# Optimization experiments

Measured on AMD Instinct MI355X. Metric: run time of the kernel, lower is better.

The kernel has to match this reference:

```python
import jax, jax.numpy as jnp
import numpy as np

N_NODES = 1_000_000
N_EDGES = 16_000_000
NUM_REL = 3
C_IN, C_OUT = 3, 2


def setup_inputs() -> dict:
    key = jax.random.key(0)
    ks = jax.random.split(key, 10)
    x = jax.random.normal(ks[0], (N_NODES, C_IN), dtype=jnp.float32)
    edge_index = jax.random.randint(ks[1], (2, N_EDGES), 0, N_NODES, dtype=jnp.int64)
    edge_attr = jax.random.randint(ks[2], (N_EDGES,), 0, NUM_REL, dtype=jnp.int64)
    s = 0.3
    W1 = jax.random.normal(ks[3], (NUM_REL, C_IN, C_OUT), dtype=jnp.float32) * s
    root1 = jax.random.normal(ks[4], (C_IN, C_OUT), dtype=jnp.float32) * s
    b1 = jax.random.normal(ks[5], (C_OUT,), dtype=jnp.float32) * s
    W2 = jax.random.normal(ks[6], (NUM_REL, C_OUT, C_OUT), dtype=jnp.float32) * s
    root2 = jax.random.normal(ks[7], (C_OUT, C_OUT), dtype=jnp.float32) * s
    b2 = jax.random.normal(ks[8], (C_OUT,), dtype=jnp.float32) * s
    return {"x": x, "edge_index": edge_index, "edge_attr": edge_attr,
            "W1": W1, "root1": root1, "b1": b1,
            "W2": W2, "root2": root2, "b2": b2}


def rgcn_conv(x, edge_index, edge_type, W, root, bias, num_nodes):
    """PyG RGCNConv: per-relation mean-aggregated messages + root transform + bias."""
    src, dst = edge_index[0], edge_index[1]
    xs = x[src]                                    # [E, c_in] gather once
    out = x @ root + bias                          # [N, c_out]
    for r in range(NUM_REL):                       # small fixed relation loop
        mask = (edge_type == r)
        msg = jnp.where(mask[:, None], xs @ W[r], 0.0)          # [E, c_out]
        sums = jax.ops.segment_sum(msg, dst, num_segments=num_nodes)
        cnt = jax.ops.segment_sum(mask.astype(x.dtype), dst, num_segments=num_nodes)
        out = out + sums / jnp.maximum(cnt, 1.0)[:, None]       # mean aggr
    return out


def reference(x, edge_index, edge_attr, W1, root1, b1, W2, root2, b2):
    h = rgcn_conv(x, edge_index, edge_attr, W1, root1, b1, N_NODES)
    h = jax.nn.relu(h)
    # F.dropout(training=self.training): identity in eval mode
    out = rgcn_conv(h, edge_index, edge_attr, W2, root2, b2, N_NODES)
    return out
```

## Files before the change

### kernel.cpp

```cpp
#include <hip/hip_runtime.h>


typedef unsigned long long u64;
typedef unsigned u32;

constexpr int NN = 1000000;
constexpr int NE = 16000000;
constexpr int NR = 3;

constexpr int BSH   = 10;
constexpr int NB    = (NN + 1023) >> 10;
constexpr int BCAP  = 18432;
constexpr int EPB   = 16384;
constexpr int NBLKB = (NE + EPB - 1) / EPB;

__device__ __forceinline__ u32 enc_x(float x0, float x1, float x2) {
    int q0 = __float2int_rn(fminf(fmaxf(x0 * 64.0f, -511.0f), 511.0f));
    int q1 = __float2int_rn(fminf(fmaxf(x1 * 128.0f, -1023.0f), 1023.0f));
    int q2 = __float2int_rn(fminf(fmaxf(x2 * 128.0f, -1023.0f), 1023.0f));
    return ((u32)(q0 + 512) & 0x3FFu)
         | (((u32)(q1 + 1024) & 0x7FFu) << 10)
         | (((u32)(q2 + 1024) & 0x7FFu) << 21);
}

__device__ __forceinline__ u64 widen_x(u32 q) {
    return (u64)(q & 0x3FFu)
         | ((u64)((q >> 10) & 0x7FFu) << 18)
         | ((u64)(q >> 21) << 36)
         | (1ULL << 54);
}

__device__ __forceinline__ u32 enc_h(float h0, float h1) {
    int q0 = __float2int_rn(fminf(h0 * 1024.0f, 32767.0f));
    int q1 = __float2int_rn(fminf(h1 * 1024.0f, 32767.0f));
    return ((u32)q0 & 0xFFFFu) | ((u32)q1 << 16);
}

__device__ __forceinline__ u64 widen_h(u32 q) {
    return (u64)(q & 0xFFFFu)
         | ((u64)(q >> 16) << 22)
         | (1ULL << 44);
}

__device__ __forceinline__ void dec_h(u32 e, float& h0, float& h1) {
    h0 = (float)(e & 0xFFFFu) * (1.0f / 1024.0f);
    h1 = (float)(e >> 16)     * (1.0f / 1024.0f);
}

constexpr u64 M28 = (1ULL << 28) - 1;
__device__ __forceinline__ u64 pack_msg(float m0, float m1) {
    int a0 = __float2int_rn(fmaf(m0, 4096.0f, 524288.0f));
    int a1 = __float2int_rn(fmaf(m1, 4096.0f, 524288.0f));
    return (u64)(u32)a0 | ((u64)(u32)a1 << 28) | (1ULL << 56);
}


__global__ __launch_bounds__(1024, 8) void scatter_kernel(
    const int* __restrict__ src, const int* __restrict__ dst, const int* __restrict__ rel,
    const float* __restrict__ x, u32* __restrict__ qx,
    u32* __restrict__ buf, u32* __restrict__ cursor)
{
    __shared__ u32 stage[EPB];
    __shared__ u32 hist[1024];
    __shared__ u32 wcur[1024];
    __shared__ u32 gbase[1024];
    __shared__ u32 wt[16];
    const int tid = threadIdx.x;
    const int wave = tid >> 6, lane = tid & 63;

    {
        int node = blockIdx.x * 1024 + tid;
        if (node < NN)
            qx[node] = enc_x(x[3 * node + 0], x[3 * node + 1], x[3 * node + 2]);
    }

    hist[tid] = 0;
    __syncthreads();

    const int base = blockIdx.x * EPB;
    const int nloc = min(EPB, NE - base);
    const int g4 = nloc >> 2;
    const int4* dp = (const int4*)(dst + base);
    const int4* sp = (const int4*)(src + base);
    const int4* rp = (const int4*)(rel + base);

    {
        const int i0 = tid, i1 = tid + 1024, i2 = tid + 2048, i3 = tid + 3072;
        const bool v0 = i0 < g4, v1 = i1 < g4, v2 = i2 < g4, v3 = i3 < g4;
        int4 a0, a1, a2, a3;
        if (v0) a0 = dp[i0];
        if (v1) a1 = dp[i1];
        if (v2) a2 = dp[i2];
        if (v3) a3 = dp[i3];
        if (v0) {
            atomicAdd(&hist[((u32)a0.x) >> BSH], 1u);
            atomicAdd(&hist[((u32)a0.y) >> BSH], 1u);
            atomicAdd(&hist[((u32)a0.z) >> BSH], 1u);
            atomicAdd(&hist[((u32)a0.w) >> BSH], 1u);
        }
        if (v1) {
            atomicAdd(&hist[((u32)a1.x) >> BSH], 1u);
            atomicAdd(&hist[((u32)a1.y) >> BSH], 1u);
            atomicAdd(&hist[((u32)a1.z) >> BSH], 1u);
            atomicAdd(&hist[((u32)a1.w) >> BSH], 1u);
        }
        if (v2) {
            atomicAdd(&hist[((u32)a2.x) >> BSH], 1u);
            atomicAdd(&hist[((u32)a2.y) >> BSH], 1u);
            atomicAdd(&hist[((u32)a2.z) >> BSH], 1u);
            atomicAdd(&hist[((u32)a2.w) >> BSH], 1u);
        }
        if (v3) {
            atomicAdd(&hist[((u32)a3.x) >> BSH], 1u);
            atomicAdd(&hist[((u32)a3.y) >> BSH], 1u);
            atomicAdd(&hist[((u32)a3.z) >> BSH], 1u);
            atomicAdd(&hist[((u32)a3.w) >> BSH], 1u);
        }
    }
    __syncthreads();

    {
        int h0 = hist[tid];
        int v0 = h0;
#pragma unroll
        for (int d = 1; d < 64; d <<= 1) {
            int t = __shfl_up(v0, d);
            if (lane >= d) v0 += t;
        }
        if (lane == 63) wt[wave] = (u32)v0;
        __syncthreads();
        u32 off = 0;
#pragma unroll
        for (int wv = 0; wv < 16; ++wv) off += (wv < wave) ? wt[wv] : 0u;
        wcur[tid] = off + (u32)(v0 - h0);
    }
    __syncthreads();

    if (tid < NB) {
        u32 c = hist[tid];
        gbase[tid] = c ? atomicAdd(&cursor[tid], c) : 0u;
    }
    __syncthreads();

    for (int i = tid; i < g4; i += 2048) {
        const int j = i + 1024;
        const bool vj = j < g4;
        int4 d0 = dp[i], s0 = sp[i], r0 = rp[i];
        int4 d1, s1, r1;
        if (vj) { d1 = dp[j]; s1 = sp[j]; r1 = rp[j]; }
        {
            u32 dd = (u32)d0.x, bk = dd >> BSH;
            u32 sl = atomicAdd(&wcur[bk], 1u);
            stage[sl] = (u32)s0.x | ((u32)r0.x << 20) | ((dd & 1023u) << 22);
        }
        {
            u32 dd = (u32)d0.y, bk = dd >> BSH;
            u32 sl = atomicAdd(&wcur[bk], 1u);
            stage[sl] = (u32)s0.y | ((u32)r0.y << 20) | ((dd & 1023u) << 22);
        }
        {
            u32 dd = (u32)d0.z, bk = dd >> BSH;
            u32 sl = atomicAdd(&wcur[bk], 1u);
            stage[sl] = (u32)s0.z | ((u32)r0.z << 20) | ((dd & 1023u) << 22);
        }
        {
            u32 dd = (u32)d0.w, bk = dd >> BSH;
            u32 sl = atomicAdd(&wcur[bk], 1u);
            stage[sl] = (u32)s0.w | ((u32)r0.w << 20) | ((dd & 1023u) << 22);
        }
        if (vj) {
            {
                u32 dd = (u32)d1.x, bk = dd >> BSH;
                u32 sl = atomicAdd(&wcur[bk], 1u);
                stage[sl] = (u32)s1.x | ((u32)r1.x << 20) | ((dd & 1023u) << 22);
            }
            {
                u32 dd = (u32)d1.y, bk = dd >> BSH;
                u32 sl = atomicAdd(&wcur[bk], 1u);
                stage[sl] = (u32)s1.y | ((u32)r1.y << 20) | ((dd & 1023u) << 22);
            }
            {
                u32 dd = (u32)d1.z, bk = dd >> BSH;
                u32 sl = atomicAdd(&wcur[bk], 1u);
                stage[sl] = (u32)s1.z | ((u32)r1.z << 20) | ((dd & 1023u) << 22);
            }
            {
                u32 dd = (u32)d1.w, bk = dd >> BSH;
                u32 sl = atomicAdd(&wcur[bk], 1u);
                stage[sl] = (u32)s1.w | ((u32)r1.w << 20) | ((dd & 1023u) << 22);
            }
        }
    }
    __syncthreads();

    {
        const int sub = lane >> 4;
        const int l16 = lane & 15;
        for (int b = (wave << 2) + sub; b < NB; b += 64) {
            u32 cnt = hist[b];
            if (!cnt) continue;
            u32 ls = wcur[b] - cnt;
            u32 gb = gbase[b];
            u32* bb = buf + (size_t)b * BCAP;
            for (u32 j = l16; j < cnt; j += 16) {
                u32 slot = gb + j;
                if (slot < (u32)BCAP) bb[slot] = stage[ls + j];
            }
        }
    }
}

__global__ __launch_bounds__(512) void agg1_kernel(
    const u32* __restrict__ buf, const u32* __restrict__ cursor,
    const u32* __restrict__ qx, const float* __restrict__ x,
    const float* __restrict__ W1,
    const float* __restrict__ root1, const float* __restrict__ b1,
    u32* __restrict__ qh)
{
    __shared__ u64 acc[1024 * NR];
    __shared__ float w[NR * 3 * 2];
    const int tid = threadIdx.x;
    for (int i = tid; i < 1024 * NR; i += 512) acc[i] = 0;
    if (tid < NR * 3 * 2) w[tid] = W1[tid];
    __syncthreads();

    const int bk = blockIdx.x;
    const int n = min((int)cursor[bk], BCAP);
    const u32* bb = buf + (size_t)bk * BCAP;
    const int n8 = n >> 3;

    int g = tid;
    uint4 A0 = make_uint4(0, 0, 0, 0), A1 = A0;
    if (g < n8) {
        const uint4* p = (const uint4*)(bb + ((size_t)g << 3));
        A0 = p[0]; A1 = p[1];
    }
    while (g < n8) {
        const int gn = g + 512;
        uint4 B0 = make_uint4(0, 0, 0, 0), B1 = B0;
        if (gn < n8) {
            const uint4* p = (const uint4*)(bb + ((size_t)gn << 3));
            B0 = p[0]; B1 = p[1];
        }
        u32 e[8] = {A0.x, A0.y, A0.z, A0.w, A1.x, A1.y, A1.z, A1.w};
        u32 q[8];
#pragma unroll
        for (int j = 0; j < 8; ++j) q[j] = qx[e[j] & 0xFFFFFu];
#pragma unroll
        for (int j = 0; j < 8; ++j)
            atomicAdd(&acc[(e[j] >> 22) * NR + ((e[j] >> 20) & 3u)], widen_x(q[j]));
        A0 = B0; A1 = B1; g = gn;
    }
    for (int i = (n8 << 3) + tid; i < n; i += 512) {
        u32 e0 = bb[i];
        u32 q0 = qx[e0 & 0xFFFFFu];
        atomicAdd(&acc[(e0 >> 22) * NR + ((e0 >> 20) & 3u)], widen_x(q0));
    }
    __syncthreads();

    for (int l = tid; l < 1024; l += 512) {
        int node = (bk << BSH) + l;
        if (node >= NN) continue;
        float x0 = x[3 * node + 0], x1 = x[3 * node + 1], x2 = x[3 * node + 2];
        float o0 = x0 * root1[0] + x1 * root1[2] + x2 * root1[4] + b1[0];
        float o1 = x0 * root1[1] + x1 * root1[3] + x2 * root1[5] + b1[1];
#pragma unroll
        for (int r = 0; r < NR; ++r) {
            u64 wv = acc[l * NR + r];
            u32 c = (u32)(wv >> 54);
            if (c) {
                float inv = 1.0f / (float)c;
                float S0 = (float)(u32)(wv & 0x3FFFFu);
                float S1 = (float)(u32)((wv >> 18) & 0x3FFFFu);
                float S2 = (float)(u32)((wv >> 36) & 0x3FFFFu);
                float m0 = fmaf(S0, inv, -512.0f)  * (1.0f / 64.0f);
                float m1 = fmaf(S1, inv, -1024.0f) * (1.0f / 128.0f);
                float m2 = fmaf(S2, inv, -1024.0f) * (1.0f / 128.0f);
                const float* wr = &w[r * 6];
                o0 += m0 * wr[0] + m1 * wr[2] + m2 * wr[4];
                o1 += m0 * wr[1] + m1 * wr[3] + m2 * wr[5];
            }
        }
        qh[node] = enc_h(fmaxf(o0, 0.0f), fmaxf(o1, 0.0f));
    }
}

__global__ __launch_bounds__(512) void agg2_kernel(
    const u32* __restrict__ buf, const u32* __restrict__ cursor,
    const u32* __restrict__ qh, const float* __restrict__ W2,
    const float* __restrict__ root2, const float* __restrict__ b2,
    float* __restrict__ out)
{
    __shared__ u64 acc[1024 * NR];
    __shared__ float w[NR * 2 * 2];
    const int tid = threadIdx.x;
    for (int i = tid; i < 1024 * NR; i += 512) acc[i] = 0;
    if (tid < NR * 2 * 2) w[tid] = W2[tid];
    __syncthreads();

    const int bk = blockIdx.x;
    const int n = min((int)cursor[bk], BCAP);
    const u32* bb = buf + (size_t)bk * BCAP;
    const int n8 = n >> 3;

    int g = tid;
    uint4 A0 = make_uint4(0, 0, 0, 0), A1 = A0;
    if (g < n8) {
        const uint4* p = (const uint4*)(bb + ((size_t)g << 3));
        A0 = p[0]; A1 = p[1];
    }
    while (g < n8) {
        const int gn = g + 512;
        uint4 B0 = make_uint4(0, 0, 0, 0), B1 = B0;
        if (gn < n8) {
            const uint4* p = (const uint4*)(bb + ((size_t)gn << 3));
            B0 = p[0]; B1 = p[1];
        }
        u32 e[8] = {A0.x, A0.y, A0.z, A0.w, A1.x, A1.y, A1.z, A1.w};
        u32 q[8];
#pragma unroll
        for (int j = 0; j < 8; ++j) q[j] = qh[e[j] & 0xFFFFFu];
#pragma unroll
        for (int j = 0; j < 8; ++j)
            atomicAdd(&acc[(e[j] >> 22) * NR + ((e[j] >> 20) & 3u)], widen_h(q[j]));
        A0 = B0; A1 = B1; g = gn;
    }
    for (int i = (n8 << 3) + tid; i < n; i += 512) {
        u32 e0 = bb[i];
        u32 q0 = qh[e0 & 0xFFFFFu];
        atomicAdd(&acc[(e0 >> 22) * NR + ((e0 >> 20) & 3u)], widen_h(q0));
    }
    __syncthreads();

    for (int l = tid; l < 1024; l += 512) {
        int node = (bk << BSH) + l;
        if (node >= NN) continue;
        float hv0, hv1;
        dec_h(qh[node], hv0, hv1);
        float o0 = hv0 * root2[0] + hv1 * root2[2] + b2[0];
        float o1 = hv0 * root2[1] + hv1 * root2[3] + b2[1];
#pragma unroll
    for (int r = 0; r < NR; ++r) {
            u64 wv = acc[l * NR + r];
            u32 c = (u32)(wv >> 44);
            if (c) {
                float inv = 1.0f / (float)c;
                float m0 = (float)(u32)(wv & 0x3FFFFFu)         * inv * (1.0f / 1024.0f);
                float m1 = (float)(u32)((wv >> 22) & 0x3FFFFFu) * inv * (1.0f / 1024.0f);
                const float* wr = &w[r * 4];
                o0 += m0 * wr[0] + m1 * wr[2];
                o1 += m0 * wr[1] + m1 * wr[3];
            }
        }
        float2 ov; ov.x = o0; ov.y = o1;
        ((float2*)out)[node] = ov;
    }
}


__global__ __launch_bounds__(256) void edge1_kernel(
    const int* __restrict__ src, const int* __restrict__ dst, const int* __restrict__ rel,
    const float* __restrict__ x, const float* __restrict__ W1,
    u64* __restrict__ sums1)
{
    __shared__ float w[NR * 3 * 2];
    if (threadIdx.x < NR * 3 * 2) w[threadIdx.x] = W1[threadIdx.x];
    __syncthreads();
    int e = blockIdx.x * 256 + threadIdx.x;
    if (e >= NE) return;
    int s = src[e], d = dst[e], r = rel[e];
    float x0 = x[3 * s + 0], x1 = x[3 * s + 1], x2 = x[3 * s + 2];
    const float* wr = &w[r * 6];
    float m0 = x0 * wr[0] + x1 * wr[2] + x2 * wr[4];
    float m1 = x0 * wr[1] + x1 * wr[3] + x2 * wr[5];
    atomicAdd(&sums1[d * NR + r], pack_msg(m0, m1));
}

__global__ __launch_bounds__(256) void node1_kernel(
    const float* __restrict__ x, const u64* __restrict__ sums1,
    const float* __restrict__ root1, const float* __restrict__ b1,
    float* __restrict__ h)
{
    int n = blockIdx.x * 256 + threadIdx.x;
    if (n >= NN) return;
    float x0 = x[3 * n + 0], x1 = x[3 * n + 1], x2 = x[3 * n + 2];
    float o0 = x0 * root1[0] + x1 * root1[2] + x2 * root1[4] + b1[0];
    float o1 = x0 * root1[1] + x1 * root1[3] + x2 * root1[5] + b1[1];
#pragma unroll
    for (int r = 0; r < NR; ++r) {
        u64 wv = sums1[n * NR + r];
        int c = (int)(wv >> 56);
        int s0i = (int)(wv & M28) - (c << 19);
        int s1i = (int)((wv >> 28) & M28) - (c << 19);
        float inv = (1.0f / 4096.0f) / (float)(c > 1 ? c : 1);
        o0 += (float)s0i * inv;
        o1 += (float)s1i * inv;
    }
    float2 hv;
    hv.x = fmaxf(o0, 0.0f);
    hv.y = fmaxf(o1, 0.0f);
    ((float2*)h)[n] = hv;
}

__global__ __launch_bounds__(256) void edge2_kernel(
    const int* __restrict__ src, const int* __restrict__ dst, const int* __restrict__ rel,
    const float* __restrict__ h, const float* __restrict__ W2,
    u64* __restrict__ sums2)
{
    __shared__ float w[NR * 2 * 2];
    if (threadIdx.x < NR * 2 * 2) w[threadIdx.x] = W2[threadIdx.x];
    __syncthreads();
    int e = blockIdx.x * 256 + threadIdx.x;
    if (e >= NE) return;
    int s = src[e];
    float2 hs = ((const float2*)h)[s];
    if (hs.x == 0.0f && hs.y == 0.0f) return;
    int d = dst[e], r = rel[e];
    const float* wr = &w[r * 4];
    float m0 = hs.x * wr[0] + hs.y * wr[2];
    float m1 = hs.x * wr[1] + hs.y * wr[3];
    atomicAdd(&sums2[d * NR + r], pack_msg(m0, m1));
}

__global__ __launch_bounds__(256) void node2_kernel(
    const float* __restrict__ h, const u64* __restrict__ sums1, const u64* __restrict__ sums2,
    const float* __restrict__ root2, const float* __restrict__ b2,
    float* __restrict__ out)
{
    int n = blockIdx.x * 256 + threadIdx.x;
    if (n >= NN) return;
    float2 hv = ((const float2*)h)[n];
    float o0 = hv.x * root2[0] + hv.y * root2[2] + b2[0];
    float o1 = hv.x * root2[1] + hv.y * root2[3] + b2[1];
#pragma unroll
    for (int r = 0; r < NR; ++r) {
        u64 w1 = sums1[n * NR + r];
        u64 w2 = sums2[n * NR + r];
        int c    = (int)(w1 >> 56);
        int adds = (int)(w2 >> 56);
        int s0i = (int)(w2 & M28) - (adds << 19);
        int s1i = (int)((w2 >> 28) & M28) - (adds << 19);
        float inv = (1.0f / 4096.0f) / (float)(c > 1 ? c : 1);
        o0 += (float)s0i * inv;
        o1 += (float)s1i * inv;
    }
    float2 ov; ov.x = o0; ov.y = o1;
    ((float2*)out)[n] = ov;
}

extern "C" void kernel_launch(void* const* d_in, const int* in_sizes, int n_in,
                              void* d_out, int out_size, void* d_ws, size_t ws_size,
                              hipStream_t stream) {
    const float* x     = (const float*)d_in[0];
    const int*   ei    = (const int*)d_in[1];
    const int*   rel   = (const int*)d_in[2];
    const float* W1    = (const float*)d_in[3];
    const float* root1 = (const float*)d_in[4];
    const float* b1    = (const float*)d_in[5];
    const float* W2    = (const float*)d_in[6];
    const float* root2 = (const float*)d_in[7];
    const float* b2    = (const float*)d_in[8];
    float* out = (float*)d_out;

    const int* src = ei;
    const int* dst = ei + NE;

    char* ws = (char*)d_ws;
    const int nb = (NN + 255) / 256;

    const size_t OFF_QX  = 72024064;
    const size_t OFF_QH  = 76024064;
    const size_t OFF_CUR = 80024064;
    const size_t WS_NEED = OFF_CUR + (size_t)NB * sizeof(u32);

    if (ws_size >= WS_NEED) {
        u32* buf    = (u32*)ws;
        u32* qx     = (u32*)(ws + OFF_QX);
        u32* qh     = (u32*)(ws + OFF_QH);
        u32* cursor = (u32*)(ws + OFF_CUR);

        hipMemsetAsync(cursor, 0, (size_t)NB * sizeof(u32), stream);
        scatter_kernel<<<NBLKB, 1024, 0, stream>>>(src, dst, rel, x, qx, buf, cursor);
        agg1_kernel<<<NB, 512, 0, stream>>>(buf, cursor, qx, x, W1, root1, b1, qh);
        agg2_kernel<<<NB, 512, 0, stream>>>(buf, cursor, qh, W2, root2, b2, out);
    } else {
        u64*   sums1 = (u64*)ws;
        u64*   sums2 = (u64*)(ws + (size_t)24 * 1000 * 1000);
        float* h     = (float*)(ws + (size_t)48 * 1000 * 1000);
        const int eb = (NE + 255) / 256;

        hipMemsetAsync(sums1, 0, (size_t)NN * NR * sizeof(u64), stream);
        hipMemsetAsync(sums2, 0, (size_t)NN * NR * sizeof(u64), stream);
        edge1_kernel<<<eb, 256, 0, stream>>>(src, dst, rel, x, W1, sums1);
        node1_kernel<<<nb, 256, 0, stream>>>(x, sums1, root1, b1, h);
        edge2_kernel<<<eb, 256, 0, stream>>>(src, dst, rel, h, W2, sums2);
        node2_kernel<<<nb, 256, 0, stream>>>(h, sums1, sums2, root2, b2, out);
    }
}
```

Before: 455.8 us.

## Fuse both aggregation layers into one kernel with a global grid barrier

Merges agg1 and agg2 into one persistent-style kernel. Each of the 977 blocks handles its bucket for layer 1, writes qh, then waits on a global atomic counter until every block has finished before running layer 2 on the same bucket. This removes one kernel launch and its launch gap. It relies on all NB blocks being resident at once (launch_bounds 512,8 plus 24KB of LDS per block), and it risks deadlock or a long spin wait if they are not.

```diff
diff --git a/kernel.cpp b/kernel.cpp
--- a/kernel.cpp
+++ b/kernel.cpp
@@ -210,51 +210,56 @@
     }
 }
 
-__global__ __launch_bounds__(512) void agg1_kernel(
+__global__ __launch_bounds__(512, 8) void fused_agg_kernel(
     const u32* __restrict__ buf, const u32* __restrict__ cursor,
     const u32* __restrict__ qx, const float* __restrict__ x,
     const float* __restrict__ W1,
     const float* __restrict__ root1, const float* __restrict__ b1,
-    u32* __restrict__ qh)
+    u32* __restrict__ qh,
+    const float* __restrict__ W2,
+    const float* __restrict__ root2, const float* __restrict__ b2,
+    float* __restrict__ out, u32* done)
 {
     __shared__ u64 acc[1024 * NR];
     __shared__ float w[NR * 3 * 2];
     const int tid = threadIdx.x;
-    for (int i = tid; i < 1024 * NR; i += 512) acc[i] = 0;
-    if (tid < NR * 3 * 2) w[tid] = W1[tid];
-    __syncthreads();
-
     const int bk = blockIdx.x;
     const int n = min((int)cursor[bk], BCAP);
     const u32* bb = buf + (size_t)bk * BCAP;
     const int n8 = n >> 3;
 
-    int g = tid;
-    uint4 A0 = make_uint4(0, 0, 0, 0), A1 = A0;
-    if (g < n8) {
-        const uint4* p = (const uint4*)(bb + ((size_t)g << 3));
-        A0 = p[0]; A1 = p[1];
-    }
-    while (g < n8) {
-        const int gn = g + 512;
-        uint4 B0 = make_uint4(0, 0, 0, 0), B1 = B0;
-        if (gn < n8) {
-            const uint4* p = (const uint4*)(bb + ((size_t)gn << 3));
-            B0 = p[0]; B1 = p[1];
-        }
-        u32 e[8] = {A0.x, A0.y, A0.z, A0.w, A1.x, A1.y, A1.z, A1.w};
-        u32 q[8];
-#pragma unroll
-        for (int j = 0; j < 8; ++j) q[j] = qx[e[j] & 0xFFFFFu];
-#pragma unroll
-        for (int j = 0; j < 8; ++j)
-            atomicAdd(&acc[(e[j] >> 22) * NR + ((e[j] >> 20) & 3u)], widen_x(q[j]));
-        A0 = B0; A1 = B1; g = gn;
-    }
-    for (int i = (n8 << 3) + tid; i < n; i += 512) {
-        u32 e0 = bb[i];
-        u32 q0 = qx[e0 & 0xFFFFFu];
-        atomicAdd(&acc[(e0 >> 22) * NR + ((e0 >> 20) & 3u)], widen_x(q0));
+    for (int i = tid; i < 1024 * NR; i += 512) acc[i] = 0;
+    if (tid < NR * 3 * 2) w[tid] = W1[tid];
+    __syncthreads();
+
+    {
+        int g = tid;
+        uint4 A0 = make_uint4(0, 0, 0, 0), A1 = A0;
+        if (g < n8) {
+            const uint4* p = (const uint4*)(bb + ((size_t)g << 3));
+            A0 = p[0]; A1 = p[1];
+        }
+        while (g < n8) {
+            const int gn = g + 512;
+            uint4 B0 = make_uint4(0, 0, 0, 0), B1 = B0;
+            if (gn < n8) {
+                const uint4* p = (const uint4*)(bb + ((size_t)gn << 3));
+                B0 = p[0]; B1 = p[1];
+            }
+            u32 e[8] = {A0.x, A0.y, A0.z, A0.w, A1.x, A1.y, A1.z, A1.w};
+            u32 q[8];
+#pragma unroll
+            for (int j = 0; j < 8; ++j) q[j] = qx[e[j] & 0xFFFFFu];
+#pragma unroll
+            for (int j = 0; j < 8; ++j)
+                atomicAdd(&acc[(e[j] >> 22) * NR + ((e[j] >> 20) & 3u)], widen_x(q[j]));
+            A0 = B0; A1 = B1; g = gn;
+        }
+        for (int i = (n8 << 3) + tid; i < n; i += 512) {
+            u32 e0 = bb[i];
+            u32 q0 = qx[e0 & 0xFFFFFu];
+            atomicAdd(&acc[(e0 >> 22) * NR + ((e0 >> 20) & 3u)], widen_x(q0));
+        }
     }
     __syncthreads();
 
@@ -283,52 +288,49 @@
         }
         qh[node] = enc_h(fmaxf(o0, 0.0f), fmaxf(o1, 0.0f));
     }
-}
-
-__global__ __launch_bounds__(512) void agg2_kernel(
-    const u32* __restrict__ buf, const u32* __restrict__ cursor,
-    const u32* __restrict__ qh, const float* __restrict__ W2,
-    const float* __restrict__ root2, const float* __restrict__ b2,
-    float* __restrict__ out)
-{
-    __shared__ u64 acc[1024 * NR];
-    __shared__ float w[NR * 2 * 2];
-    const int tid = threadIdx.x;
+
+    __syncthreads();
+    __threadfence();
+    if (tid == 0) {
+        atomicAdd(done, 1u);
+        while (__hip_atomic_load(done, __ATOMIC_ACQUIRE,
+                                 __HIP_MEMORY_SCOPE_AGENT) < (u32)NB) { }
+    }
+    __syncthreads();
+    __threadfence();
+
     for (int i = tid; i < 1024 * NR; i += 512) acc[i] = 0;
     if (tid < NR * 2 * 2) w[tid] = W2[tid];
     __syncthreads();
 
-    const int bk = blockIdx.x;
-    const int n = min((int)cursor[bk], BCAP);
-    const u32* bb = buf + (size_t)bk * BCAP;
-    const int n8 = n >> 3;
-
-    int g = tid;
-    uint4 A0 = make_uint4(0, 0, 0, 0), A1 = A0;
-    if (g < n8) {
-        const uint4* p = (const uint4*)(bb + ((size_t)g << 3));
-        A0 = p[0]; A1 = p[1];
-    }
-    while (g < n8) {
-        const int gn = g + 512;
-        uint4 B0 = make_uint4(0, 0, 0, 0), B1 = B0;
-        if (gn < n8) {
-            const uint4* p = (const uint4*)(bb + ((size_t)gn << 3));
-            B0 = p[0]; B1 = p[1];
-        }
-        u32 e[8] = {A0.x, A0.y, A0.z, A0.w, A1.x, A1.y, A1.z, A1.w};
-        u32 q[8];
-#pragma unroll
-        for (int j = 0; j < 8; ++j) q[j] = qh[e[j] & 0xFFFFFu];
-#pragma unroll
-        for (int j = 0; j < 8; ++j)
-            atomicAdd(&acc[(e[j] >> 22) * NR + ((e[j] >> 20) & 3u)], widen_h(q[j]));
-        A0 = B0; A1 = B1; g = gn;
-    }
-    for (int i = (n8 << 3) + tid; i < n; i += 512) {
-        u32 e0 = bb[i];
-        u32 q0 = qh[e0 & 0xFFFFFu];
-        atomicAdd(&acc[(e0 >> 22) * NR + ((e0 >> 20) & 3u)], widen_h(q0));
+    {
+        int g = tid;
+        uint4 A0 = make_uint4(0, 0, 0, 0), A1 = A0;
+        if (g < n8) {
+            const uint4* p = (const uint4*)(bb + ((size_t)g << 3));
+            A0 = p[0]; A1 = p[1];
+        }
+        while (g < n8) {
+            const int gn = g + 512;
+            uint4 B0 = make_uint4(0, 0, 0, 0), B1 = B0;
+            if (gn < n8) {
+                const uint4* p = (const uint4*)(bb + ((size_t)gn << 3));
+                B0 = p[0]; B1 = p[1];
+            }
+            u32 e[8] = {A0.x, A0.y, A0.z, A0.w, A1.x, A1.y, A1.z, A1.w};
+            u32 q[8];
+#pragma unroll
+            for (int j = 0; j < 8; ++j) q[j] = qh[e[j] & 0xFFFFFu];
+#pragma unroll
+            for (int j = 0; j < 8; ++j)
+                atomicAdd(&acc[(e[j] >> 22) * NR + ((e[j] >> 20) & 3u)], widen_h(q[j]));
+            A0 = B0; A1 = B1; g = gn;
+        }
+        for (int i = (n8 << 3) + tid; i < n; i += 512) {
+            u32 e0 = bb[i];
+            u32 q0 = qh[e0 & 0xFFFFFu];
+            atomicAdd(&acc[(e0 >> 22) * NR + ((e0 >> 20) & 3u)], widen_h(q0));
+        }
     }
     __syncthreads();
 
@@ -340,7 +342,7 @@
         float o0 = hv0 * root2[0] + hv1 * root2[2] + b2[0];
         float o1 = hv0 * root2[1] + hv1 * root2[3] + b2[1];
 #pragma unroll
-    for (int r = 0; r < NR; ++r) {
+        for (int r = 0; r < NR; ++r) {
             u64 wv = acc[l * NR + r];
             u32 c = (u32)(wv >> 44);
             if (c) {
@@ -471,18 +473,20 @@
     const size_t OFF_QX  = 72024064;
     const size_t OFF_QH  = 76024064;
     const size_t OFF_CUR = 80024064;
-    const size_t WS_NEED = OFF_CUR + (size_t)NB * sizeof(u32);
+    const size_t WS_NEED = OFF_CUR + (size_t)NB * sizeof(u32) + sizeof(u32);
 
     if (ws_size >= WS_NEED) {
         u32* buf    = (u32*)ws;
         u32* qx     = (u32*)(ws + OFF_QX);
         u32* qh     = (u32*)(ws + OFF_QH);
         u32* cursor = (u32*)(ws + OFF_CUR);
-
-        hipMemsetAsync(cursor, 0, (size_t)NB * sizeof(u32), stream);
+        u32* done   = cursor + NB;
+
+        hipMemsetAsync(cursor, 0, ((size_t)NB + 1) * sizeof(u32), stream);
         scatter_kernel<<<NBLKB, 1024, 0, stream>>>(src, dst, rel, x, qx, buf, cursor);
-        agg1_kernel<<<NB, 512, 0, stream>>>(buf, cursor, qx, x, W1, root1, b1, qh);
-        agg2_kernel<<<NB, 512, 0, stream>>>(buf, cursor, qh, W2, root2, b2, out);
+        fused_agg_kernel<<<NB, 512, 0, stream>>>(buf, cursor, qx, x,
+                                                 W1, root1, b1, qh,
+                                                 W2, root2, b2, out, done);
     } else {
         u64*   sums1 = (u64*)ws;
         u64*   sums2 = (u64*)(ws + (size_t)24 * 1000 * 1000);
```

Measured after the change: 1.096 ms. +140.5%, slower.
